# Kernel tuning notes

Measured on AMD Instinct MI355X. Metric: run time of the kernel, lower is better.

Reference implementation:

```python
import jax, jax.numpy as jnp
import numpy as np

B, D, E, P = 8192, 2048, 16, 1024
C0, C1 = 64, 128
LN_EPS = 1e-5
W_STD = 0.02


def _ln(x):
    # F.layer_norm over last dim, no affine params
    mu = jnp.mean(x, axis=-1, keepdims=True)
    var = jnp.var(x, axis=-1, keepdims=True)
    return (x - mu) * jax.lax.rsqrt(var + LN_EPS)


def setup_inputs() -> dict:
    key = jax.random.key(0)
    ks = jax.random.split(key, 8)
    return {
        "x": jax.random.normal(ks[0], (B, D), jnp.float32),
        "pw_fc": jax.random.normal(ks[1], (E, D), jnp.float32) * W_STD,
        "pb_fc": jnp.zeros((E,), jnp.float32),
        "pw_proj": jax.random.normal(ks[2], (P, E), jnp.float32) * W_STD,
        "pb_proj": jnp.zeros((P,), jnp.float32),
        "cw_fc0": jax.random.normal(ks[3], (E, C0, D), jnp.float32) * W_STD,
        "cb_fc0": jnp.zeros((E, C0), jnp.float32),
        "cw_proj0": jax.random.normal(ks[4], (E, P, C0), jnp.float32) * W_STD,
        "cb_proj0": jnp.zeros((E, P), jnp.float32),
        "cw_fc1": jax.random.normal(ks[5], (E, C1, D), jnp.float32) * W_STD,
        "cb_fc1": jnp.zeros((E, C1), jnp.float32),
        "cw_proj1": jax.random.normal(ks[6], (E, P, C1), jnp.float32) * W_STD,
        "cb_proj1": jnp.zeros((E, P), jnp.float32),
    }


def _child_level(x, parent_class, wfc, bfc, wproj, bproj):
    # Dense compute over all experts, then per-sample select (grouped-GEMM semantics).
    all_logits = jnp.einsum("bd,ecd->bec", x, wfc) + bfc          # [B,E,C]
    sel = jnp.take_along_axis(all_logits, parent_class[:, None, None], axis=1)[:, 0]  # [B,C]
    h = _ln(sel)                                                   # child logits (layer-normed)
    proj_all = jnp.einsum("bc,epc->bep", h, wproj) + bproj        # [B,E,P]
    proj = jnp.take_along_axis(proj_all, parent_class[:, None, None], axis=1)[:, 0]   # [B,P]
    return h, proj


def reference(x, pw_fc, pb_fc, pw_proj, pb_proj,
              cw_fc0, cb_fc0, cw_proj0, cb_proj0,
              cw_fc1, cb_fc1, cw_proj1, cb_proj1):
    # dropouts are identity (eval mode / p applied only in training)
    parent_logits = _ln(x @ pw_fc.T + pb_fc)                      # [B,E]
    parent_proj = parent_logits @ pw_proj.T + pb_proj             # [B,P]
    # argmax(softmax(z)) == argmax(z)
    parent_class = jnp.argmax(parent_logits, axis=1)              # [B]

    cl0, cp0 = _child_level(x, parent_class, cw_fc0, cb_fc0, cw_proj0, cb_proj0)
    cl1, cp1 = _child_level(x, parent_class, cw_fc1, cb_fc1, cw_proj1, cb_proj1)

    # torch returns (parent_logits, [cl0, cl1], parent_proj, [cp0, cp1]) - flattened here
    return (parent_logits, cl0, cl1, parent_proj, cp0, cp1)
```

## Files before the change

kernel.cpp:

```cpp
#include <hip/hip_runtime.h>

#define B_ 8192
#define D_ 2048
#define E_ 16
#define P_ 1024

typedef unsigned int u32;
typedef __attribute__((ext_vector_type(8)))  short bf16x8;
typedef __attribute__((ext_vector_type(16))) float f32x16;

__device__ __forceinline__ float dot4(float4 a, float4 b) {
  return a.x*b.x + a.y*b.y + a.z*b.z + a.w*b.w;
}

__device__ __forceinline__ void split2(float a, float b, u32& h, u32& l) {
  u32 ua = __float_as_uint(a), ub = __float_as_uint(b);
  h = __builtin_amdgcn_perm(ub, ua, 0x07060302u);
  float la = a - __uint_as_float(ua & 0xFFFF0000u);
  float lb = b - __uint_as_float(ub & 0xFFFF0000u);
  l = __builtin_amdgcn_perm(__float_as_uint(lb), __float_as_uint(la), 0x07060302u);
}
__device__ __forceinline__ void split8(float4 f0, float4 f1, uint4& hi, uint4& lo) {
  split2(f0.x, f0.y, hi.x, lo.x);
  split2(f0.z, f0.w, hi.y, lo.y);
  split2(f1.x, f1.y, hi.z, lo.z);
  split2(f1.z, f1.w, hi.w, lo.w);
}

__device__ __forceinline__ f32x16 mfma32(uint4 a, uint4 b, f32x16 c) {
  return __builtin_amdgcn_mfma_f32_32x32x16_bf16(
      __builtin_bit_cast(bf16x8, a), __builtin_bit_cast(bf16x8, b), c, 0, 0, 0);
}

__global__ void k_zero(int* __restrict__ counts) {
  if (threadIdx.x < 16) counts[threadIdx.x] = 0;
}

__global__ __launch_bounds__(512) void k_parent(
    const float* __restrict__ x, const float* __restrict__ wfc,
    const float* __restrict__ bfc, const float* __restrict__ wp,
    const float* __restrict__ bp, float* __restrict__ out_pl,
    float* __restrict__ out_pp, int* __restrict__ cls, int* __restrict__ counts)
{
  __shared__ float wl[16 * 512];
  __shared__ float pl_lds[32][20];
  const int tid  = threadIdx.x;
  const int wave = tid >> 6, lane = tid & 63;
  const int row0 = blockIdx.x * 32 + wave * 4;

  const int p0 = tid * 2;
  float4 wq[8];
  #pragma unroll
  for (int q = 0; q < 8; ++q) wq[q] = ((const float4*)(wp + p0 * 16))[q];
  const float bq0 = bp[p0], bq1 = bp[p0 + 1];

  float acc[4][16];
  #pragma unroll
  for (int r = 0; r < 4; ++r)
    #pragma unroll
    for (int e = 0; e < 16; ++e) acc[r][e] = 0.f;

  for (int ch = 0; ch < 4; ++ch) {
    __syncthreads();
    #pragma unroll
    for (int it = 0; it < 4; ++it) {
      int i = tid * 4 + it * 2048;
      int e = i >> 9, k = i & 511;
      *(float4*)&wl[i] = *(const float4*)&wfc[e * 2048 + ch * 512 + k];
    }
    __syncthreads();
    float4 xv[4][2];
    #pragma unroll
    for (int r = 0; r < 4; ++r) {
      const float* xr = x + (size_t)(row0 + r) * D_ + ch * 512;
      xv[r][0] = *(const float4*)&xr[lane * 4];
      xv[r][1] = *(const float4*)&xr[lane * 4 + 256];
    }
    #pragma unroll
    for (int e = 0; e < 16; ++e) {
      float4 w0 = *(const float4*)&wl[e * 512 + lane * 4];
      float4 w1 = *(const float4*)&wl[e * 512 + lane * 4 + 256];
      #pragma unroll
      for (int r = 0; r < 4; ++r)
        acc[r][e] += dot4(xv[r][0], w0) + dot4(xv[r][1], w1);
    }
  }
  #pragma unroll
  for (int r = 0; r < 4; ++r)
    #pragma unroll
    for (int e = 0; e < 16; ++e) {
      float v = acc[r][e];
      #pragma unroll
      for (int m = 32; m >= 1; m >>= 1) v += __shfl_xor(v, m, 64);
      acc[r][e] = v;
    }
  if (lane < 4) {
    const int r = lane;
    const int row = row0 + r;
    float z[16]; float s = 0.f;
    #pragma unroll
    for (int e = 0; e < 16; ++e) { z[e] = acc[r][e] + bfc[e]; s += z[e]; }
    const float mu = s * (1.f / 16.f);
    float s2 = 0.f;
    #pragma unroll
    for (int e = 0; e < 16; ++e) { float d = z[e] - mu; s2 += d * d; }
    const float rstd = rsqrtf(s2 * (1.f / 16.f) + 1e-5f);
    int best = 0; float bv = z[0];
    #pragma unroll
    for (int e = 1; e < 16; ++e) if (z[e] > bv) { bv = z[e]; best = e; }
    #pragma unroll
    for (int e = 0; e < 16; ++e) {
      const float zn = (z[e] - mu) * rstd;
      out_pl[(size_t)row * 16 + e] = zn;
      pl_lds[wave * 4 + r][e] = zn;
    }
    cls[row] = best;
    atomicAdd(&counts[best], 1);
  }
  __syncthreads();
  #pragma unroll 4
  for (int r = 0; r < 32; ++r) {
    float4 a0 = *(const float4*)&pl_lds[r][0];
    float4 a1 = *(const float4*)&pl_lds[r][4];
    float4 a2 = *(const float4*)&pl_lds[r][8];
    float4 a3 = *(const float4*)&pl_lds[r][12];
    float o0 = dot4(a0, wq[0]) + dot4(a1, wq[1]) + dot4(a2, wq[2]) + dot4(a3, wq[3]) + bq0;
    float o1 = dot4(a0, wq[4]) + dot4(a1, wq[5]) + dot4(a2, wq[6]) + dot4(a3, wq[7]) + bq1;
    float2 ov = {o0, o1};
    *(float2*)&out_pp[(size_t)(blockIdx.x * 32 + r) * 1024 + p0] = ov;
  }
}

__global__ void k_scan(const int* __restrict__ counts,
                       int* __restrict__ starts, int* __restrict__ cursor) {
  if (threadIdx.x == 0) {
    int run = 0;
    for (int e = 0; e < 16; ++e) { starts[e] = run; cursor[e] = run; run += counts[e]; }
  }
}

__global__ __launch_bounds__(256) void k_scatter(
    const int* __restrict__ cls, int* __restrict__ cursor, int* __restrict__ idxb) {
  const int b = blockIdx.x * 256 + threadIdx.x;
  const int c = cls[b];
  const int pos = atomicAdd(&cursor[c], 1);
  idxb[pos] = b;
}

template<int C>
__device__ __forceinline__ void child_body(
    char* smem, int* rid_s,
    const float* __restrict__ x, const float* __restrict__ wfc,
    const float* __restrict__ bfc, const float* __restrict__ wpj,
    const float* __restrict__ bpj, const int* __restrict__ starts,
    const int* __restrict__ counts, const int* __restrict__ idxb,
    float* __restrict__ out_cl, float* __restrict__ out_cp,
    const int e, const int t)
{
  constexpr int NFR = C / 32;
  constexpr int KS  = C / 16;
  const int tid = threadIdx.x;
  const int lane = tid & 63, wave = tid >> 6;
  const int l31 = lane & 31, lh = lane >> 5;

  const int n = counts[e];
  const int r0 = t * 64;
  if (r0 >= n) return;
  const int rows = min(64, n - r0);
  const int st = starts[e];
  if (tid < 64) rid_s[tid] = idxb[st + r0 + min(tid, rows - 1)];
  __syncthreads();

  const float* xa0 = x + (size_t)rid_s[l31] * D_ + lh * 8;
  const float* xa1 = x + (size_t)rid_s[32 + l31] * D_ + lh * 8;
  const float* wa[NFR];
  #pragma unroll
  for (int nf = 0; nf < NFR; ++nf)
    wa[nf] = wfc + (size_t)(e * C + nf * 32 + l31) * D_ + lh * 8;

  f32x16 acc[2][NFR];
  #pragma unroll
  for (int mf = 0; mf < 2; ++mf)
    #pragma unroll
    for (int nf = 0; nf < NFR; ++nf)
      #pragma unroll
      for (int r = 0; r < 16; ++r) acc[mf][nf][r] = 0.f;

  const int kbase = wave << 9;
  for (int s = 0; s < 32; ++s) {
    const int k0 = kbase + (s << 4);
    uint4 xh[2], xl[2], wh[NFR], wlo[NFR];
    {
      float4 f0 = *(const float4*)(xa0 + k0);
      float4 f1 = *(const float4*)(xa0 + k0 + 4);
      split8(f0, f1, xh[0], xl[0]);
      f0 = *(const float4*)(xa1 + k0);
      f1 = *(const float4*)(xa1 + k0 + 4);
      split8(f0, f1, xh[1], xl[1]);
    }
    #pragma unroll
    for (int nf = 0; nf < NFR; ++nf) {
      float4 f0 = *(const float4*)(wa[nf] + k0);
      float4 f1 = *(const float4*)(wa[nf] + k0 + 4);
      split8(f0, f1, wh[nf], wlo[nf]);
    }
    #pragma unroll
    for (int nf = 0; nf < NFR; ++nf)
      #pragma unroll
      for (int mf = 0; mf < 2; ++mf) {
        acc[mf][nf] = mfma32(xh[mf], wh[nf],  acc[mf][nf]);
        acc[mf][nf] = mfma32(xh[mf], wlo[nf], acc[mf][nf]);
        acc[mf][nf] = mfma32(xl[mf], wh[nf],  acc[mf][nf]);
      }
  }

  uint4* red4 = (uint4*)smem;
  #pragma unroll
  for (int mf = 0; mf < 2; ++mf) {
    __syncthreads();
    if (wave != mf) {
      const int sw = (wave < mf) ? wave : wave - 1;
      #pragma unroll
      for (int nf = 0; nf < NFR; ++nf)
        #pragma unroll
        for (int q = 0; q < 4; ++q) {
          uint4 v;
          v.x = __float_as_uint(acc[mf][nf][4 * q + 0]);
          v.y = __float_as_uint(acc[mf][nf][4 * q + 1]);
          v.z = __float_as_uint(acc[mf][nf][4 * q + 2]);
          v.w = __float_as_uint(acc[mf][nf][4 * q + 3]);
          red4[((nf * 4 + q) * 3 + sw) * 64 + lane] = v;
        }
    }
    __syncthreads();
    if (wave == mf) {
      #pragma unroll
      for (int nf = 0; nf < NFR; ++nf)
        #pragma unroll
        for (int q = 0; q < 4; ++q)
          #pragma unroll
          for (int sw = 0; sw < 3; ++sw) {
            uint4 v = red4[((nf * 4 + q) * 3 + sw) * 64 + lane];
            acc[mf][nf][4 * q + 0] += __uint_as_float(v.x);
            acc[mf][nf][4 * q + 1] += __uint_as_float(v.y);
            acc[mf][nf][4 * q + 2] += __uint_as_float(v.z);
            acc[mf][nf][4 * q + 3] += __uint_as_float(v.w);
          }
    }
  }
  __syncthreads();

  float* hbuf = (float*)smem;
  if (wave < 2) {
    const int mf = wave;
    float h[NFR][16];
    #pragma unroll
    for (int nf = 0; nf < NFR; ++nf) {
      const float bias = bfc[e * C + nf * 32 + l31];
      #pragma unroll
      for (int r = 0; r < 16; ++r) h[nf][r] = acc[mf][nf][r] + bias;
    }
    #pragma unroll
    for (int r = 0; r < 16; ++r) {
      float sv = 0.f, qv = 0.f;
      #pragma unroll
      for (int nf = 0; nf < NFR; ++nf) { sv += h[nf][r]; qv += h[nf][r] * h[nf][r]; }
      #pragma unroll
      for (int m = 1; m < 32; m <<= 1) { sv += __shfl_xor(sv, m, 64); qv += __shfl_xor(qv, m, 64); }
      const float mu = sv * (1.f / C);
      const float var = qv * (1.f / C) - mu * mu;
      const float rstd = rsqrtf(var + 1e-5f);
      const int row_l = mf * 32 + (r & 3) + 8 * (r >> 2) + 4 * lh;
      const bool valid = row_l < rows;
      const int rid = rid_s[row_l];
      #pragma unroll
      for (int nf = 0; nf < NFR; ++nf) {
        const float hn = (h[nf][r] - mu) * rstd;
        h[nf][r] = hn;
        if (valid) out_cl[(size_t)rid * C + nf * 32 + l31] = hn;
        hbuf[row_l * (C + 4) + nf * 32 + l31] = hn;
      }
    }
  }
  __syncthreads();

  uint4 pah[2][KS], pal[2][KS];
  #pragma unroll
  for (int mf = 0; mf < 2; ++mf)
    #pragma unroll
    for (int ks = 0; ks < KS; ++ks) {
      const float* hp = hbuf + (mf * 32 + l31) * (C + 4) + ks * 16 + lh * 8;
      float4 f0 = *(const float4*)hp;
      float4 f1 = *(const float4*)(hp + 4);
      split8(f0, f1, pah[mf][ks], pal[mf][ks]);
    }

  #pragma unroll 1
  for (int j = 0; j < 8; ++j) {
    const int nfg = wave * 8 + j;
    const float* wb = wpj + (size_t)(e * 1024 + nfg * 32 + l31) * C + lh * 8;
    f32x16 p[2];
    #pragma unroll
    for (int mf = 0; mf < 2; ++mf)
      #pragma unroll
      for (int r = 0; r < 16; ++r) p[mf][r] = 0.f;
    #pragma unroll
    for (int ks = 0; ks < KS; ++ks) {
      float4 f0 = *(const float4*)(wb + ks * 16);
      float4 f1 = *(const float4*)(wb + ks * 16 + 4);
      uint4 wh, wlo;
      split8(f0, f1, wh, wlo);
      #pragma unroll
      for (int mf = 0; mf < 2; ++mf) {
        p[mf] = mfma32(pah[mf][ks], wh,  p[mf]);
        p[mf] = mfma32(pah[mf][ks], wlo, p[mf]);
        p[mf] = mfma32(pal[mf][ks], wh,  p[mf]);
      }
    }
    const float bias = bpj[e * 1024 + nfg * 32 + l31];
    #pragma unroll
    for (int mf = 0; mf < 2; ++mf)
      #pragma unroll
      for (int r = 0; r < 16; ++r) {
        const int row_l = mf * 32 + (r & 3) + 8 * (r >> 2) + 4 * lh;
        if (row_l < rows)
          out_cp[(size_t)rid_s[row_l] * 1024 + nfg * 32 + l31] = p[mf][r] + bias;
      }
  }
}

__global__ __launch_bounds__(256, 1) void k_child_both(
    const float* __restrict__ x,
    const float* __restrict__ wfc0, const float* __restrict__ bfc0,
    const float* __restrict__ wpj0, const float* __restrict__ bpj0,
    const float* __restrict__ wfc1, const float* __restrict__ bfc1,
    const float* __restrict__ wpj1, const float* __restrict__ bpj1,
    const int* __restrict__ starts, const int* __restrict__ counts,
    const int* __restrict__ idxb,
    float* __restrict__ out_cl0, float* __restrict__ out_cp0,
    float* __restrict__ out_cl1, float* __restrict__ out_cp1)
{
  __shared__ __align__(16) char smem[49152];
  __shared__ int rid_s[64];
  const int e = blockIdx.x & 15;
  const int rest = blockIdx.x >> 4;
  const int lvl = rest & 1;
  const int t = rest >> 1;
  if (lvl == 0)
    child_body<64>(smem, rid_s, x, wfc0, bfc0, wpj0, bpj0,
                   starts, counts, idxb, out_cl0, out_cp0, e, t);
  else
    child_body<128>(smem, rid_s, x, wfc1, bfc1, wpj1, bpj1,
                    starts, counts, idxb, out_cl1, out_cp1, e, t);
}

extern "C" void kernel_launch(void* const* d_in, const int* in_sizes, int n_in,
                              void* d_out, int out_size, void* d_ws, size_t ws_size,
                              hipStream_t stream)
{
  (void)in_sizes; (void)n_in; (void)out_size; (void)ws_size;
  const float* x       = (const float*)d_in[0];
  const float* pw_fc   = (const float*)d_in[1];
  const float* pb_fc   = (const float*)d_in[2];
  const float* pw_proj = (const float*)d_in[3];
  const float* pb_proj = (const float*)d_in[4];
  const float* cw_fc0  = (const float*)d_in[5];
  const float* cb_fc0  = (const float*)d_in[6];
  const float* cw_pj0  = (const float*)d_in[7];
  const float* cb_pj0  = (const float*)d_in[8];
  const float* cw_fc1  = (const float*)d_in[9];
  const float* cb_fc1  = (const float*)d_in[10];
  const float* cw_pj1  = (const float*)d_in[11];
  const float* cb_pj1  = (const float*)d_in[12];

  float* out = (float*)d_out;
  float* out_pl  = out;
  float* out_cl0 = out_pl  + (size_t)B_ * 16;
  float* out_cl1 = out_cl0 + (size_t)B_ * 64;
  float* out_pp  = out_cl1 + (size_t)B_ * 128;
  float* out_cp0 = out_pp  + (size_t)B_ * 1024;
  float* out_cp1 = out_cp0 + (size_t)B_ * 1024;

  int* cls    = (int*)d_ws;
  int* idxb   = cls + B_;
  int* counts = idxb + B_;
  int* starts = counts + 16;
  int* cursor = starts + 16;

  k_zero<<<1, 64, 0, stream>>>(counts);
  k_parent<<<256, 512, 0, stream>>>(x, pw_fc, pb_fc, pw_proj, pb_proj,
                                    out_pl, out_pp, cls, counts);
  k_scan<<<1, 64, 0, stream>>>(counts, starts, cursor);
  k_scatter<<<B_ / 256, 256, 0, stream>>>(cls, cursor, idxb);
  k_child_both<<<4096, 256, 0, stream>>>(
      x, cw_fc0, cb_fc0, cw_pj0, cb_pj0, cw_fc1, cb_fc1, cw_pj1, cb_pj1,
      starts, counts, idxb, out_cl0, out_cp0, out_cl1, out_cp1);
}
```

Baseline: 520.8 us.

## Shrink child tiles to 32 rows with 512-thread split-K blocks and prefetch

The child kernel moves from 64-row tiles on 256 threads to 32-row tiles on 512 threads. Waves are split across output column groups and K-slices, with partial sums reduced through shared memory, and each wave keeps one accumulator and prefetches its next K chunk in registers. The parent kernel halves its rows per block and doubles its grid, and both kernels get occupancy launch bounds. The aim is more waves and more blocks in flight to hide memory latency. The cost is that weight rows are re-read by twice as many tiles, and there are extra LDS reductions and barriers.

```diff
diff --git a/kernel.cpp b/kernel.cpp
--- a/kernel.cpp
+++ b/kernel.cpp
@@ -2,8 +2,6 @@
 
 #define B_ 8192
 #define D_ 2048
-#define E_ 16
-#define P_ 1024
 
 typedef unsigned int u32;
 typedef __attribute__((ext_vector_type(8)))  short bf16x8;
@@ -36,17 +34,17 @@
   if (threadIdx.x < 16) counts[threadIdx.x] = 0;
 }
 
-__global__ __launch_bounds__(512) void k_parent(
+__global__ __launch_bounds__(512, 4) void k_parent(
     const float* __restrict__ x, const float* __restrict__ wfc,
     const float* __restrict__ bfc, const float* __restrict__ wp,
     const float* __restrict__ bp, float* __restrict__ out_pl,
     float* __restrict__ out_pp, int* __restrict__ cls, int* __restrict__ counts)
 {
   __shared__ float wl[16 * 512];
-  __shared__ float pl_lds[32][20];
+  __shared__ float pl_lds[16][20];
   const int tid  = threadIdx.x;
   const int wave = tid >> 6, lane = tid & 63;
-  const int row0 = blockIdx.x * 32 + wave * 4;
+  const int row0 = blockIdx.x * 16 + wave * 2;
 
   const int p0 = tid * 2;
   float4 wq[8];
@@ -54,9 +52,9 @@
   for (int q = 0; q < 8; ++q) wq[q] = ((const float4*)(wp + p0 * 16))[q];
   const float bq0 = bp[p0], bq1 = bp[p0 + 1];
 
-  float acc[4][16];
-  #pragma unroll
-  for (int r = 0; r < 4; ++r)
+  float acc[2][16];
+  #pragma unroll
+  for (int r = 0; r < 2; ++r)
     #pragma unroll
     for (int e = 0; e < 16; ++e) acc[r][e] = 0.f;
 
@@ -69,9 +67,9 @@
       *(float4*)&wl[i] = *(const float4*)&wfc[e * 2048 + ch * 512 + k];
     }
     __syncthreads();
-    float4 xv[4][2];
-    #pragma unroll
-    for (int r = 0; r < 4; ++r) {
+    float4 xv[2][2];
+    #pragma unroll
+    for (int r = 0; r < 2; ++r) {
       const float* xr = x + (size_t)(row0 + r) * D_ + ch * 512;
       xv[r][0] = *(const float4*)&xr[lane * 4];
       xv[r][1] = *(const float4*)&xr[lane * 4 + 256];
@@ -81,12 +79,12 @@
       float4 w0 = *(const float4*)&wl[e * 512 + lane * 4];
       float4 w1 = *(const float4*)&wl[e * 512 + lane * 4 + 256];
       #pragma unroll
-      for (int r = 0; r < 4; ++r)
+      for (int r = 0; r < 2; ++r)
         acc[r][e] += dot4(xv[r][0], w0) + dot4(xv[r][1], w1);
     }
   }
   #pragma unroll
-  for (int r = 0; r < 4; ++r)
+  for (int r = 0; r < 2; ++r)
     #pragma unroll
     for (int e = 0; e < 16; ++e) {
       float v = acc[r][e];
@@ -94,7 +92,7 @@
       for (int m = 32; m >= 1; m >>= 1) v += __shfl_xor(v, m, 64);
       acc[r][e] = v;
     }
-  if (lane < 4) {
+  if (lane < 2) {
     const int r = lane;
     const int row = row0 + r;
     float z[16]; float s = 0.f;
@@ -112,14 +110,14 @@
     for (int e = 0; e < 16; ++e) {
       const float zn = (z[e] - mu) * rstd;
       out_pl[(size_t)row * 16 + e] = zn;
-      pl_lds[wave * 4 + r][e] = zn;
+      pl_lds[wave * 2 + r][e] = zn;
     }
     cls[row] = best;
     atomicAdd(&counts[best], 1);
   }
   __syncthreads();
   #pragma unroll 4
-  for (int r = 0; r < 32; ++r) {
+  for (int r = 0; r < 16; ++r) {
     float4 a0 = *(const float4*)&pl_lds[r][0];
     float4 a1 = *(const float4*)&pl_lds[r][4];
     float4 a2 = *(const float4*)&pl_lds[r][8];
@@ -127,7 +125,7 @@
     float o0 = dot4(a0, wq[0]) + dot4(a1, wq[1]) + dot4(a2, wq[2]) + dot4(a3, wq[3]) + bq0;
     float o1 = dot4(a0, wq[4]) + dot4(a1, wq[5]) + dot4(a2, wq[6]) + dot4(a3, wq[7]) + bq1;
     float2 ov = {o0, o1};
-    *(float2*)&out_pp[(size_t)(blockIdx.x * 32 + r) * 1024 + p0] = ov;
+    *(float2*)&out_pp[(size_t)(blockIdx.x * 16 + r) * 1024 + p0] = ov;
   }
 }
 
@@ -149,7 +147,7 @@
 
 template<int C>
 __device__ __forceinline__ void child_body(
-    char* smem, int* rid_s,
+    float* smemf, int* rid_s, float* snm,
     const float* __restrict__ x, const float* __restrict__ wfc,
     const float* __restrict__ bfc, const float* __restrict__ wpj,
     const float* __restrict__ bpj, const int* __restrict__ starts,
@@ -157,179 +155,141 @@
     float* __restrict__ out_cl, float* __restrict__ out_cp,
     const int e, const int t)
 {
-  constexpr int NFR = C / 32;
-  constexpr int KS  = C / 16;
+  constexpr int NG = C / 32;
+  constexpr int KSPL = 8 / NG;
+  constexpr int KSTEPS = 128 / KSPL;
+  constexpr int KS = C / 16;
   const int tid = threadIdx.x;
   const int lane = tid & 63, wave = tid >> 6;
   const int l31 = lane & 31, lh = lane >> 5;
+  const int ng = wave % NG, kq = wave / NG;
 
   const int n = counts[e];
-  const int r0 = t * 64;
+  const int r0 = t * 32;
   if (r0 >= n) return;
-  const int rows = min(64, n - r0);
-  const int st = starts[e];
-  if (tid < 64) rid_s[tid] = idxb[st + r0 + min(tid, rows - 1)];
-  __syncthreads();
-
-  const float* xa0 = x + (size_t)rid_s[l31] * D_ + lh * 8;
-  const float* xa1 = x + (size_t)rid_s[32 + l31] * D_ + lh * 8;
-  const float* wa[NFR];
-  #pragma unroll
-  for (int nf = 0; nf < NFR; ++nf)
-    wa[nf] = wfc + (size_t)(e * C + nf * 32 + l31) * D_ + lh * 8;
-
-  f32x16 acc[2][NFR];
-  #pragma unroll
-  for (int mf = 0; mf < 2; ++mf)
-    #pragma unroll
-    for (int nf = 0; nf < NFR; ++nf)
-      #pragma unroll
-      for (int r = 0; r < 16; ++r) acc[mf][nf][r] = 0.f;
-
-  const int kbase = wave << 9;
-  for (int s = 0; s < 32; ++s) {
-    const int k0 = kbase + (s << 4);
-    uint4 xh[2], xl[2], wh[NFR], wlo[NFR];
-    {
-      float4 f0 = *(const float4*)(xa0 + k0);
-      float4 f1 = *(const float4*)(xa0 + k0 + 4);
-      split8(f0, f1, xh[0], xl[0]);
-      f0 = *(const float4*)(xa1 + k0);
-      f1 = *(const float4*)(xa1 + k0 + 4);
-      split8(f0, f1, xh[1], xl[1]);
-    }
-    #pragma unroll
-    for (int nf = 0; nf < NFR; ++nf) {
-      float4 f0 = *(const float4*)(wa[nf] + k0);
-      float4 f1 = *(const float4*)(wa[nf] + k0 + 4);
-      split8(f0, f1, wh[nf], wlo[nf]);
-    }
-    #pragma unroll
-    for (int nf = 0; nf < NFR; ++nf)
-      #pragma unroll
-      for (int mf = 0; mf < 2; ++mf) {
-        acc[mf][nf] = mfma32(xh[mf], wh[nf],  acc[mf][nf]);
-        acc[mf][nf] = mfma32(xh[mf], wlo[nf], acc[mf][nf]);
-        acc[mf][nf] = mfma32(xl[mf], wh[nf],  acc[mf][nf]);
+  const int rows = min(32, n - r0);
+  if (tid < 32) rid_s[tid] = idxb[starts[e] + r0 + min(tid, rows - 1)];
+  __syncthreads();
+
+  const float* xa = x + (size_t)rid_s[l31] * D_ + lh * 8;
+  const float* wa = wfc + (size_t)(e * C + ng * 32 + l31) * D_ + lh * 8;
+  const int kbase = kq * (KSTEPS * 16);
+
+  f32x16 acc;
+  #pragma unroll
+  for (int r = 0; r < 16; ++r) acc[r] = 0.f;
+
+  float4 a0 = *(const float4*)(xa + kbase);
+  float4 a1 = *(const float4*)(xa + kbase + 4);
+  float4 b0 = *(const float4*)(wa + kbase);
+  float4 b1 = *(const float4*)(wa + kbase + 4);
+  for (int s = 0; s < KSTEPS; ++s) {
+    float4 na0, na1, nb0, nb1;
+    if (s + 1 < KSTEPS) {
+      const int kn = kbase + (s + 1) * 16;
+      na0 = *(const float4*)(xa + kn);
+      na1 = *(const float4*)(xa + kn + 4);
+      nb0 = *(const float4*)(wa + kn);
+      nb1 = *(const float4*)(wa + kn + 4);
+    }
+    uint4 xh, xl, wh, wl2;
+    split8(a0, a1, xh, xl);
+    split8(b0, b1, wh, wl2);
+    acc = mfma32(xh, wh,  acc);
+    acc = mfma32(xh, wl2, acc);
+    acc = mfma32(xl, wh,  acc);
+    a0 = na0; a1 = na1; b0 = nb0; b1 = nb1;
+  }
+
+  __syncthreads();
+  if (kq > 0) {
+    float* p = smemf + ((ng * (KSPL - 1) + (kq - 1)) * 64 + lane) * 17;
+    #pragma unroll
+    for (int r = 0; r < 16; ++r) p[r] = acc[r];
+  }
+  __syncthreads();
+
+  float h[16];
+  if (kq == 0) {
+    #pragma unroll
+    for (int sl = 0; sl < KSPL - 1; ++sl) {
+      const float* p = smemf + ((ng * (KSPL - 1) + sl) * 64 + lane) * 17;
+      #pragma unroll
+      for (int r = 0; r < 16; ++r) acc[r] += p[r];
+    }
+    const float bias = bfc[e * C + ng * 32 + l31];
+    #pragma unroll
+    for (int r = 0; r < 16; ++r) h[r] = acc[r] + bias;
+    #pragma unroll
+    for (int r = 0; r < 16; ++r) {
+      float sv = h[r], qv = h[r] * h[r];
+      #pragma unroll
+      for (int m = 1; m < 32; m <<= 1) { sv += __shfl_xor(sv, m, 64); qv += __shfl_xor(qv, m, 64); }
+      if (l31 == 0) {
+        const int row = (r & 3) + 8 * (r >> 2) + 4 * lh;
+        snm[(ng * 32 + row) * 2 + 0] = sv;
+        snm[(ng * 32 + row) * 2 + 1] = qv;
       }
-  }
-
-  uint4* red4 = (uint4*)smem;
-  #pragma unroll
-  for (int mf = 0; mf < 2; ++mf) {
-    __syncthreads();
-    if (wave != mf) {
-      const int sw = (wave < mf) ? wave : wave - 1;
-      #pragma unroll
-      for (int nf = 0; nf < NFR; ++nf)
-        #pragma unroll
-        for (int q = 0; q < 4; ++q) {
-          uint4 v;
-          v.x = __float_as_uint(acc[mf][nf][4 * q + 0]);
-          v.y = __float_as_uint(acc[mf][nf][4 * q + 1]);
-          v.z = __float_as_uint(acc[mf][nf][4 * q + 2]);
-          v.w = __float_as_uint(acc[mf][nf][4 * q + 3]);
-          red4[((nf * 4 + q) * 3 + sw) * 64 + lane] = v;
-        }
-    }
-    __syncthreads();
-    if (wave == mf) {
-      #pragma unroll
-      for (int nf = 0; nf < NFR; ++nf)
-        #pragma unroll
-        for (int q = 0; q < 4; ++q)
-          #pragma unroll
-          for (int sw = 0; sw < 3; ++sw) {
-            uint4 v = red4[((nf * 4 + q) * 3 + sw) * 64 + lane];
-            acc[mf][nf][4 * q + 0] += __uint_as_float(v.x);
-            acc[mf][nf][4 * q + 1] += __uint_as_float(v.y);
-            acc[mf][nf][4 * q + 2] += __uint_as_float(v.z);
-            acc[mf][nf][4 * q + 3] += __uint_as_float(v.w);
-          }
-    }
-  }
-  __syncthreads();
-
-  float* hbuf = (float*)smem;
-  if (wave < 2) {
-    const int mf = wave;
-    float h[NFR][16];
-    #pragma unroll
-    for (int nf = 0; nf < NFR; ++nf) {
-      const float bias = bfc[e * C + nf * 32 + l31];
-      #pragma unroll
-      for (int r = 0; r < 16; ++r) h[nf][r] = acc[mf][nf][r] + bias;
-    }
+    }
+  }
+  __syncthreads();
+
+  float* hbuf = smemf;
+  if (kq == 0) {
     #pragma unroll
     for (int r = 0; r < 16; ++r) {
-      float sv = 0.f, qv = 0.f;
-      #pragma unroll
-      for (int nf = 0; nf < NFR; ++nf) { sv += h[nf][r]; qv += h[nf][r] * h[nf][r]; }
-      #pragma unroll
-      for (int m = 1; m < 32; m <<= 1) { sv += __shfl_xor(sv, m, 64); qv += __shfl_xor(qv, m, 64); }
-      const float mu = sv * (1.f / C);
-      const float var = qv * (1.f / C) - mu * mu;
+      const int row = (r & 3) + 8 * (r >> 2) + 4 * lh;
+      float S = 0.f, Q = 0.f;
+      #pragma unroll
+      for (int g = 0; g < NG; ++g) {
+        S += snm[(g * 32 + row) * 2 + 0];
+        Q += snm[(g * 32 + row) * 2 + 1];
+      }
+      const float mu = S * (1.f / C);
+      const float var = Q * (1.f / C) - mu * mu;
       const float rstd = rsqrtf(var + 1e-5f);
-      const int row_l = mf * 32 + (r & 3) + 8 * (r >> 2) + 4 * lh;
-      const bool valid = row_l < rows;
-      const int rid = rid_s[row_l];
-      #pragma unroll
-      for (int nf = 0; nf < NFR; ++nf) {
-        const float hn = (h[nf][r] - mu) * rstd;
-        h[nf][r] = hn;
-        if (valid) out_cl[(size_t)rid * C + nf * 32 + l31] = hn;
-        hbuf[row_l * (C + 4) + nf * 32 + l31] = hn;
-      }
-    }
-  }
-  __syncthreads();
-
-  uint4 pah[2][KS], pal[2][KS];
-  #pragma unroll
-  for (int mf = 0; mf < 2; ++mf)
-    #pragma unroll
-    for (int ks = 0; ks < KS; ++ks) {
-      const float* hp = hbuf + (mf * 32 + l31) * (C + 4) + ks * 16 + lh * 8;
-      float4 f0 = *(const float4*)hp;
-      float4 f1 = *(const float4*)(hp + 4);
-      split8(f0, f1, pah[mf][ks], pal[mf][ks]);
-    }
-
-  #pragma unroll 1
-  for (int j = 0; j < 8; ++j) {
-    const int nfg = wave * 8 + j;
-    const float* wb = wpj + (size_t)(e * 1024 + nfg * 32 + l31) * C + lh * 8;
-    f32x16 p[2];
-    #pragma unroll
-    for (int mf = 0; mf < 2; ++mf)
-      #pragma unroll
-      for (int r = 0; r < 16; ++r) p[mf][r] = 0.f;
+      const float hn = (h[r] - mu) * rstd;
+      const int col = ng * 32 + l31;
+      if (row < rows) out_cl[(size_t)rid_s[row] * C + col] = hn;
+      hbuf[row * (C + 4) + col] = hn;
+    }
+  }
+  __syncthreads();
+
+  uint4 pah[KS], pal[KS];
+  #pragma unroll
+  for (int ks = 0; ks < KS; ++ks) {
+    const float* hp = hbuf + l31 * (C + 4) + ks * 16 + lh * 8;
+    split8(*(const float4*)hp, *(const float4*)(hp + 4), pah[ks], pal[ks]);
+  }
+
+  for (int j = 0; j < 4; ++j) {
+    const int p32 = j * 8 + wave;
+    const float* wb = wpj + (size_t)(e * 1024 + p32 * 32 + l31) * C + lh * 8;
+    f32x16 p;
+    #pragma unroll
+    for (int r = 0; r < 16; ++r) p[r] = 0.f;
     #pragma unroll
     for (int ks = 0; ks < KS; ++ks) {
       float4 f0 = *(const float4*)(wb + ks * 16);
       float4 f1 = *(const float4*)(wb + ks * 16 + 4);
-      uint4 wh, wlo;
-      split8(f0, f1, wh, wlo);
-      #pragma unroll
-      for (int mf = 0; mf < 2; ++mf) {
-        p[mf] = mfma32(pah[mf][ks], wh,  p[mf]);
-        p[mf] = mfma32(pah[mf][ks], wlo, p[mf]);
-        p[mf] = mfma32(pal[mf][ks], wh,  p[mf]);
-      }
-    }
-    const float bias = bpj[e * 1024 + nfg * 32 + l31];
-    #pragma unroll
-    for (int mf = 0; mf < 2; ++mf)
-      #pragma unroll
-      for (int r = 0; r < 16; ++r) {
-        const int row_l = mf * 32 + (r & 3) + 8 * (r >> 2) + 4 * lh;
-        if (row_l < rows)
-          out_cp[(size_t)rid_s[row_l] * 1024 + nfg * 32 + l31] = p[mf][r] + bias;
-      }
-  }
-}
-
-__global__ __launch_bounds__(256, 1) void k_child_both(
+      uint4 wh, wl2;
+      split8(f0, f1, wh, wl2);
+      p = mfma32(pah[ks], wh,  p);
+      p = mfma32(pah[ks], wl2, p);
+      p = mfma32(pal[ks], wh,  p);
+    }
+    const float bias = bpj[e * 1024 + p32 * 32 + l31];
+    #pragma unroll
+    for (int r = 0; r < 16; ++r) {
+      const int row = (r & 3) + 8 * (r >> 2) + 4 * lh;
+      if (row < rows)
+        out_cp[(size_t)rid_s[row] * 1024 + p32 * 32 + l31] = p[r] + bias;
+    }
+  }
+}
+
+__global__ __launch_bounds__(512, 4) void k_child_both(
     const float* __restrict__ x,
     const float* __restrict__ wfc0, const float* __restrict__ bfc0,
     const float* __restrict__ wpj0, const float* __restrict__ bpj0,
@@ -340,17 +300,17 @@
     float* __restrict__ out_cl0, float* __restrict__ out_cp0,
     float* __restrict__ out_cl1, float* __restrict__ out_cp1)
 {
-  __shared__ __align__(16) char smem[49152];
-  __shared__ int rid_s[64];
+  __shared__ __align__(16) float smemf[6528];
+  __shared__ int rid_s[32];
+  __shared__ float snm[4 * 32 * 2];
   const int e = blockIdx.x & 15;
-  const int rest = blockIdx.x >> 4;
-  const int lvl = rest & 1;
-  const int t = rest >> 1;
+  const int lvl = (blockIdx.x >> 4) & 1;
+  const int t = blockIdx.x >> 5;
   if (lvl == 0)
-    child_body<64>(smem, rid_s, x, wfc0, bfc0, wpj0, bpj0,
+    child_body<64>(smemf, rid_s, snm, x, wfc0, bfc0, wpj0, bpj0,
                    starts, counts, idxb, out_cl0, out_cp0, e, t);
   else
-    child_body<128>(smem, rid_s, x, wfc1, bfc1, wpj1, bpj1,
+    child_body<128>(smemf, rid_s, snm, x, wfc1, bfc1, wpj1, bpj1,
                     starts, counts, idxb, out_cl1, out_cp1, e, t);
 }
 
@@ -388,11 +348,11 @@
   int* cursor = starts + 16;
 
   k_zero<<<1, 64, 0, stream>>>(counts);
-  k_parent<<<256, 512, 0, stream>>>(x, pw_fc, pb_fc, pw_proj, pb_proj,
+  k_parent<<<512, 512, 0, stream>>>(x, pw_fc, pb_fc, pw_proj, pb_proj,
                                     out_pl, out_pp, cls, counts);
   k_scan<<<1, 64, 0, stream>>>(counts, starts, cursor);
   k_scatter<<<B_ / 256, 256, 0, stream>>>(cls, cursor, idxb);
-  k_child_both<<<4096, 256, 0, stream>>>(
+  k_child_both<<<8192, 512, 0, stream>>>(
       x, cw_fc0, cb_fc0, cw_pj0, cb_pj0, cw_fc1, cb_fc1, cw_pj1, cb_pj1,
       starts, counts, idxb, out_cl0, out_cp0, out_cl1, out_cp1);
 }
```

After: 520.8 us. About the same (+0.0%).
